# Performance work log

Measured on AMD Instinct MI355X. Metric: run time of the kernel, lower is better.

The kernel has to match this reference:

```python
import jax, jax.numpy as jnp
import numpy as np

D, H, B, NSTEPS = 128, 512, 128, 16


def setup_inputs() -> dict:
    key = jax.random.key(0)
    k0, k1, k2, k3 = jax.random.split(key, 4)
    s1 = 1.0 / np.sqrt(D)
    s2 = 0.1 / np.sqrt(H)  # small output scale keeps the flow well-conditioned
    return {
        "x0": jax.random.normal(k0, (B, D), jnp.float32),
        "W1": jax.random.normal(k1, (D, H), jnp.float32) * s1,
        "b1": jnp.zeros((H,), jnp.float32),
        "u1": jax.random.normal(k2, (H,), jnp.float32) * 0.1,
        "W2": jax.random.normal(k3, (H, D), jnp.float32) * s2,
        "b2": jnp.zeros((D,), jnp.float32),
        "n_steps": NSTEPS,
    }


def reference(x0, W1, b1, u1, W2, b2, n_steps):
    d = x0.shape[-1]
    LOG2PI = float(np.log(2.0 * np.pi))
    # log prob of x0 under standard-normal prior p0
    log_px0 = -0.5 * jnp.sum(x0 * x0, axis=-1) - 0.5 * d * LOG2PI
    dt = 1.0 / n_steps

    sg = jax.lax.stop_gradient
    W1s, b1s, u1s, W2s, b2s = sg(W1), sg(b1), sg(u1), sg(W2), sg(b2)

    def vf(t, x, w1, c1, v1, w2, c2):  # time-conditioned MLP vector field, x: (d,)
        return jnp.tanh(x @ w1 + c1 + t * v1) @ w2 + c2

    eye = jnp.eye(d, dtype=x0.dtype)

    def f_single(t, x):
        # exact Jacobian trace via vmapped JVP over identity tangents (stop-grad params)
        apply_sg = lambda xx: vf(t, xx, W1s, b1s, u1s, W2s, b2s)
        jvp1 = lambda e: jax.jvp(apply_sg, (x,), (e,))[1]
        jac = jax.vmap(jvp1)(eye)              # (d, d)
        dxdt = vf(t, x, W1, b1, u1, W2, b2)    # with grad-carrying params
        dlogpxdt = -jnp.trace(jac)
        gradlogpx = -x                          # grad log of standard-normal target
        dkldt = -jnp.vdot(gradlogpx, dxdt) + dlogpxdt
        return dxdt, dlogpxdt, dkldt

    rhs = jax.vmap(f_single, in_axes=(None, 0))  # batch over samples

    # Dopri5 Butcher tableau (fixed-step 5th-order solution)
    A = (
        (1 / 5,),
        (3 / 40, 9 / 40),
        (44 / 45, -56 / 15, 32 / 9),
        (19372 / 6561, -25360 / 2187, 64448 / 6561, -212 / 729),
        (9017 / 3168, -355 / 33, 46732 / 5247, 49 / 176, -5103 / 18656),
    )
    C = (1 / 5, 3 / 10, 4 / 5, 8 / 9, 1.0)
    BW = (35 / 384, 0.0, 500 / 1113, 125 / 192, -2187 / 6784, 11 / 84)

    def lin(y, ks, cs):  # y + dt * sum(c_i * k_i), tree-structured state
        return jax.tree_util.tree_map(
            lambda yv, *kv: yv + dt * sum(c * k for c, k in zip(cs, kv)), y, *ks)

    def step(y, t):
        ks = [rhs(t, y[0])]
        for ai, ci in zip(A, C):
            yi = lin(y, ks, ai)
            ks.append(rhs(t + ci * dt, yi[0]))
        return lin(y, ks, BW), None

    nb = x0.shape[0]
    y0 = (x0, jnp.zeros((nb,), x0.dtype), jnp.zeros((nb,), x0.dtype))
    ts = jnp.arange(n_steps, dtype=x0.dtype) * dt
    (z, log_det, kl), _ = jax.lax.scan(step, y0, ts)
    log_px = log_px0 + log_det
    return z, log_px, kl
```

## Files before the change

### kernel.cpp

```cpp
#include <hip/hip_runtime.h>

#define TPB 512

typedef _Float16 hf2 __attribute__((ext_vector_type(2)));

__device__ __forceinline__ hf2 as_h2(unsigned u) { return __builtin_bit_cast(hf2, u); }
__device__ __forceinline__ unsigned pk2h(float a, float b) {
    unsigned la = (unsigned)__builtin_bit_cast(unsigned short, (_Float16)a);
    unsigned hb = (unsigned)__builtin_bit_cast(unsigned short, (_Float16)b);
    return la | (hb << 16);
}
__device__ __forceinline__ unsigned short h16(float a) {
    return __builtin_bit_cast(unsigned short, (_Float16)a);
}
#define FDOT2(w, x, acc) __builtin_amdgcn_fdot2(as_h2(w), as_h2(x), (acc), false)

__device__ __forceinline__ unsigned rdl(unsigned v, int l) {
    return (unsigned)__builtin_amdgcn_readlane((int)v, l);
}

#define G16(M) M(0) M(1) M(2) M(3) M(4) M(5) M(6) M(7) M(8) M(9) M(10) M(11) \
  M(12) M(13) M(14) M(15)

#define RED64(v) { v += __shfl_xor(v,32,64); v += __shfl_xor(v,16,64); \
  v += __shfl_xor(v,8,64); v += __shfl_xor(v,4,64); v += __shfl_xor(v,2,64); \
  v += __shfl_xor(v,1,64); }

__global__ __launch_bounds__(TPB, 1) void vi_node_kernel(
    const float* __restrict__ x0, const float* __restrict__ W1,
    const float* __restrict__ b1, const float* __restrict__ u1,
    const float* __restrict__ W2, const float* __restrict__ b2,
    const int* __restrict__ nsp, float* __restrict__ out, int nB)
{
    const int s    = blockIdx.x;
    const int t    = threadIdx.x;
    const int j    = t & 127;
    const int q    = t >> 7;
    const int kb   = q << 7;
    const int lane = t & 63;
    const int wid  = t >> 6;

    __shared__ uint4 W1L[16 * 512];
    __shared__ __align__(16) float    xs32[128];
    __shared__ __align__(8)  unsigned xsPK[64];
    __shared__ __align__(16) float    ys[128];
    __shared__ __align__(8)  unsigned aPK[256];
    __shared__ __align__(16) float    part[4][128];
    __shared__ __align__(16) float    kx[6][128];
    __shared__ float wredT[2][6][8];
    __shared__ float wredX[2][6][2];
    __shared__ float sqred[2];

#pragma unroll
    for (int c = 0; c < 16; ++c) {
        const float* gp = W1 + (8 * c) * 512 + t;
        uint4 wv;
        wv.x = pk2h(gp[0],        gp[512]);
        wv.y = pk2h(gp[2 * 512],  gp[3 * 512]);
        wv.z = pk2h(gp[4 * 512],  gp[5 * 512]);
        wv.w = pk2h(gp[6 * 512],  gp[7 * 512]);
        W1L[c * 512 + t] = wv;
    }

#define DECLZ(g) unsigned z_##g##_0, z_##g##_1, z_##g##_2, z_##g##_3;
    G16(DECLZ)
#define PKW2(r) pk2h(W2[(r) * 128 + j], W2[((r) + 1) * 128 + j])
#define LOADZ(g) { const int r_ = kb + 8 * (g); \
    z_##g##_0 = PKW2(r_);     z_##g##_1 = PKW2(r_ + 2); \
    z_##g##_2 = PKW2(r_ + 4); z_##g##_3 = PKW2(r_ + 6); }
    G16(LOADZ)

    const float b1k = b1[t];
    const float u1k = u1[t];
    const float b2j = b2[j];

    const int ns = nsp[0];
    const float dt = 1.f / (float)ns;

    if (t < 128) {
        float xv0 = x0[s * 128 + t];
        ys[t] = xv0;
        xs32[t] = xv0;
        ((unsigned short*)xsPK)[t] = h16(xv0);
        float sq = xv0 * xv0;
        RED64(sq)
        if (lane == 0) sqred[wid] = sq;
    }
    __syncthreads();

    float wd = 0.f;
    {
        const float4* w2r4 = (const float4*)(W2 + t * 128);
#pragma unroll
        for (int c = 0; c < 16; ++c) {
            uint4 wv = W1L[c * 512 + t];
            float4 a4 = w2r4[2 * c], b4 = w2r4[2 * c + 1];
            wd = FDOT2(wv.x, pk2h(a4.x, a4.y), wd);
            wd = FDOT2(wv.y, pk2h(a4.z, a4.w), wd);
            wd = FDOT2(wv.z, pk2h(b4.x, b4.y), wd);
            wd = FDOT2(wv.w, pk2h(b4.z, b4.w), wd);
        }
    }
    const float sumsq = sqred[0] + sqred[1];
    float ld_acc = 0.f, kl_acc = 0.f;

#define H4(c) { uint4 w_ = W1L[(c) * 512 + t]; \
    m0 = FDOT2(w_.x, rdl(xv, 4*(c)+0), m0); \
    m1 = FDOT2(w_.y, rdl(xv, 4*(c)+1), m1); \
    m2 = FDOT2(w_.z, rdl(xv, 4*(c)+2), m2); \
    m3 = FDOT2(w_.w, rdl(xv, 4*(c)+3), m3); }

#define P4(g) { \
    p0 = FDOT2(z_##g##_0, rdl(av, 4*(g)+0), p0); \
    p1 = FDOT2(z_##g##_1, rdl(av, 4*(g)+1), p1); \
    p2 = FDOT2(z_##g##_2, rdl(av, 4*(g)+2), p2); \
    p3 = FDOT2(z_##g##_3, rdl(av, 4*(g)+3), p3); }

#define K(sidx) kx[sidx][t]

#define EVAL(STAGE, TVAL, XNEW, EXTRA)                                         \
    {                                                                          \
        const unsigned xv = xsPK[lane];            \
        float m0 = 0.f, m1 = 0.f, m2 = 0.f, m3 = 0.f;                          \
        H4(0) H4(1) H4(2) H4(3) H4(4) H4(5) H4(6) H4(7)                        \
        H4(8) H4(9) H4(10) H4(11) H4(12) H4(13) H4(14) H4(15)                  \
        float hh = fmaf((TVAL), u1k, b1k) + ((m0 + m1) + (m2 + m3));           \
        float ee = __expf(2.f * hh);                                           \
        float aa = 1.f - 2.f / (ee + 1.f);                           \
        ((unsigned short*)aPK)[t] = h16(aa);                                   \
        float trp = (1.f - aa * aa) * wd;                                      \
        RED64(trp)                                                             \
        if (lane == 0) wredT[par][STAGE][wid] = trp;                           \
        __syncthreads();                            \
        const unsigned av = aPK[(q << 6) + lane];   \
        float p0 = 0.f, p1 = 0.f, p2 = 0.f, p3 = 0.f;                          \
        P4(0) P4(1) P4(2) P4(3) P4(4) P4(5) P4(6) P4(7)                        \
        P4(8) P4(9) P4(10) P4(11) P4(12) P4(13) P4(14) P4(15)                  \
        part[q][j] = (p0 + p1) + (p2 + p3);                                    \
        __syncthreads();                               \
        if (t < 128) {                                                         \
            float dx = ((part[0][t] + part[1][t]) + (part[2][t] + part[3][t])) \
                       + b2j;                                                  \
            kx[STAGE][t] = dx;                                                 \
            float xd = xs32[t] * dx;                                           \
            RED64(xd)                                                          \
            if (lane == 0) wredX[par][STAGE][wid] = xd;                        \
            float xnew = (XNEW);                                               \
            xs32[t] = xnew;                                                    \
            ((unsigned short*)xsPK)[t] = h16(xnew);                            \
            EXTRA                                                              \
        }                                                                      \
        __syncthreads();                               \
    }

    for (int n = 0; n < ns; ++n) {
        const float tn = (float)n;
        const int par = n & 1;

        EVAL(0, dt * tn,
             fmaf(dt, 0.2f * dx, ys[t]), ;)

        EVAL(1, dt * (tn + 0.2f),
             ys[t] + dt * (0.075f * K(0) + 0.225f * dx), ;)

        EVAL(2, dt * (tn + 0.3f),
             ys[t] + dt * ((float)(44.0/45.0)  * K(0) + (float)(-56.0/15.0) * K(1)
                         + (float)(32.0/9.0)   * dx), ;)

        EVAL(3, dt * (tn + 0.8f),
             ys[t] + dt * ((float)(19372.0/6561.0) * K(0) + (float)(-25360.0/2187.0) * K(1)
                         + (float)(64448.0/6561.0) * K(2) + (float)(-212.0/729.0)    * dx), ;)

        EVAL(4, dt * (tn + (float)(8.0/9.0)),
             ys[t] + dt * ((float)(9017.0/3168.0)  * K(0) + (float)(-355.0/33.0)     * K(1)
                         + (float)(46732.0/5247.0) * K(2) + (float)(49.0/176.0)      * K(3)
                         + (float)(-5103.0/18656.0)* dx), ;)

        EVAL(5, dt * (tn + 1.0f),
             ys[t] + dt * ((float)(35.0/384.0)     * K(0) + (float)(500.0/1113.0)   * K(2)
                         + (float)(125.0/192.0)    * K(3) + (float)(-2187.0/6784.0) * K(4)
                         + (float)(11.0/84.0)      * dx),
             ys[t] = xnew;)

        if (t == 0) {
#define TAILS(sidx, bw) { \
            float tr_ = ((wredT[par][sidx][0] + wredT[par][sidx][1])  \
                       + (wredT[par][sidx][2] + wredT[par][sidx][3])) \
                      + ((wredT[par][sidx][4] + wredT[par][sidx][5])  \
                       + (wredT[par][sidx][6] + wredT[par][sidx][7])); \
            float dv_ = wredX[par][sidx][0] + wredX[par][sidx][1]; \
            ld_acc += dt * (bw) * (-tr_); \
            kl_acc += dt * (bw) * (dv_ - tr_); }
            TAILS(0, (float)(35.0/384.0))
            TAILS(2, (float)(500.0/1113.0))
            TAILS(3, (float)(125.0/192.0))
            TAILS(4, (float)(-2187.0/6784.0))
            TAILS(5, (float)(11.0/84.0))
        }
    }

    if (t < 128) out[s * 128 + t] = ys[t];
    if (t == 0) {
        const float LOG2PI = 1.8378770664093454f;
        float lpx0 = -0.5f * sumsq - 0.5f * 128.f * LOG2PI;
        out[nB * 128 + s]      = lpx0 + ld_acc;
        out[nB * 128 + nB + s] = kl_acc;
    }
}

extern "C" void kernel_launch(void* const* d_in, const int* in_sizes, int n_in,
                              void* d_out, int out_size, void* d_ws, size_t ws_size,
                              hipStream_t stream) {
    const float* x0 = (const float*)d_in[0];
    const float* W1 = (const float*)d_in[1];
    const float* b1 = (const float*)d_in[2];
    const float* u1 = (const float*)d_in[3];
    const float* W2 = (const float*)d_in[4];
    const float* b2 = (const float*)d_in[5];
    const int*  nsp = (const int*)d_in[6];
    float* out = (float*)d_out;
    const int nB = in_sizes[0] / 128;

    hipLaunchKernelGGL(vi_node_kernel, dim3(nB), dim3(TPB), 0, stream,
                       x0, W1, b1, u1, W2, b2, nsp, out, nB);
}
```

Measured before the change: 255.6 us.

## Double block size and split matvec reductions across wave halves with LDS vector reads

The block grows from 512 to 1024 threads. Each hidden unit's W1 dot product is split across two half-waves and combined with a cross-lane shuffle. The W2 product is spread over 8 partial slices instead of 4, which halves the register-held W2 fragment per thread. Broadcast operands now come from vectorized LDS uint4 reads instead of scalar readlane, aiming to shorten the serial dependent chain in each stage. In exchange, only half the lanes do the tanh work, and there are more partial sums to combine and larger barriers.

Result: faster. 237.9 us (-6.9%).

```diff
diff --git a/kernel.cpp b/kernel.cpp
--- a/kernel.cpp
+++ b/kernel.cpp
@@ -1,6 +1,6 @@
 #include <hip/hip_runtime.h>
 
-#define TPB 512
+#define TPB 1024
 
 typedef _Float16 hf2 __attribute__((ext_vector_type(2)));
 
@@ -15,12 +15,7 @@
 }
 #define FDOT2(w, x, acc) __builtin_amdgcn_fdot2(as_h2(w), as_h2(x), (acc), false)
 
-__device__ __forceinline__ unsigned rdl(unsigned v, int l) {
-    return (unsigned)__builtin_amdgcn_readlane((int)v, l);
-}
-
-#define G16(M) M(0) M(1) M(2) M(3) M(4) M(5) M(6) M(7) M(8) M(9) M(10) M(11) \
-  M(12) M(13) M(14) M(15)
+#define G8(M) M(0) M(1) M(2) M(3) M(4) M(5) M(6) M(7)
 
 #define RED64(v) { v += __shfl_xor(v,32,64); v += __shfl_xor(v,16,64); \
   v += __shfl_xor(v,8,64); v += __shfl_xor(v,4,64); v += __shfl_xor(v,2,64); \
@@ -34,44 +29,51 @@
 {
     const int s    = blockIdx.x;
     const int t    = threadIdx.x;
+    const int l    = t & 63;
+    const int w    = t >> 6;
+    const int h    = 32 * w + (t & 31);
+    const int half = (t >> 5) & 1;
+    const int hb   = half * 32;
     const int j    = t & 127;
     const int q    = t >> 7;
-    const int kb   = q << 7;
-    const int lane = t & 63;
-    const int wid  = t >> 6;
 
     __shared__ uint4 W1L[16 * 512];
     __shared__ __align__(16) float    xs32[128];
-    __shared__ __align__(8)  unsigned xsPK[64];
+    __shared__ __align__(16) unsigned xsPK[64];
     __shared__ __align__(16) float    ys[128];
-    __shared__ __align__(8)  unsigned aPK[256];
-    __shared__ __align__(16) float    part[4][128];
+    __shared__ __align__(16) unsigned aPK[256];
+    __shared__ __align__(16) float    part[8][128];
     __shared__ __align__(16) float    kx[6][128];
-    __shared__ float wredT[2][6][8];
+    __shared__ float wredT[2][6][16];
     __shared__ float wredX[2][6][2];
     __shared__ float sqred[2];
 
+    {
+        const int col = t & 511;
+        const int c0  = t >> 9;
 #pragma unroll
-    for (int c = 0; c < 16; ++c) {
-        const float* gp = W1 + (8 * c) * 512 + t;
-        uint4 wv;
-        wv.x = pk2h(gp[0],        gp[512]);
-        wv.y = pk2h(gp[2 * 512],  gp[3 * 512]);
-        wv.z = pk2h(gp[4 * 512],  gp[5 * 512]);
-        wv.w = pk2h(gp[6 * 512],  gp[7 * 512]);
-        W1L[c * 512 + t] = wv;
-    }
-
-#define DECLZ(g) unsigned z_##g##_0, z_##g##_1, z_##g##_2, z_##g##_3;
-    G16(DECLZ)
+        for (int cc = 0; cc < 8; ++cc) {
+            const int c = 8 * c0 + cc;
+            const float* gp = W1 + (8 * c) * 512 + col;
+            uint4 wv;
+            wv.x = pk2h(gp[0],        gp[512]);
+            wv.y = pk2h(gp[2 * 512],  gp[3 * 512]);
+            wv.z = pk2h(gp[4 * 512],  gp[5 * 512]);
+            wv.w = pk2h(gp[6 * 512],  gp[7 * 512]);
+            W1L[c * 512 + col] = wv;
+        }
+    }
+
+#define DECLZ(cc) unsigned zc_##cc##_0, zc_##cc##_1, zc_##cc##_2, zc_##cc##_3;
+    G8(DECLZ)
 #define PKW2(r) pk2h(W2[(r) * 128 + j], W2[((r) + 1) * 128 + j])
-#define LOADZ(g) { const int r_ = kb + 8 * (g); \
-    z_##g##_0 = PKW2(r_);     z_##g##_1 = PKW2(r_ + 2); \
-    z_##g##_2 = PKW2(r_ + 4); z_##g##_3 = PKW2(r_ + 6); }
-    G16(LOADZ)
-
-    const float b1k = b1[t];
-    const float u1k = u1[t];
+#define LOADZ(cc) { const int r_ = 64 * q + 8 * (cc); \
+    zc_##cc##_0 = PKW2(r_);     zc_##cc##_1 = PKW2(r_ + 2); \
+    zc_##cc##_2 = PKW2(r_ + 4); zc_##cc##_3 = PKW2(r_ + 6); }
+    G8(LOADZ)
+
+    const float b1k = b1[h];
+    const float u1k = u1[h];
     const float b2j = b2[j];
 
     const int ns = nsp[0];
@@ -84,67 +86,70 @@
         ((unsigned short*)xsPK)[t] = h16(xv0);
         float sq = xv0 * xv0;
         RED64(sq)
-        if (lane == 0) sqred[wid] = sq;
+        if (l == 0) sqred[w] = sq;
     }
     __syncthreads();
 
-    float wd = 0.f;
+    float wd;
     {
-        const float4* w2r4 = (const float4*)(W2 + t * 128);
+        float wp = 0.f;
+        const float4* w2r4 = (const float4*)(W2 + h * 128);
 #pragma unroll
-        for (int c = 0; c < 16; ++c) {
-            uint4 wv = W1L[c * 512 + t];
-            float4 a4 = w2r4[2 * c], b4 = w2r4[2 * c + 1];
-            wd = FDOT2(wv.x, pk2h(a4.x, a4.y), wd);
-            wd = FDOT2(wv.y, pk2h(a4.z, a4.w), wd);
-            wd = FDOT2(wv.z, pk2h(b4.x, b4.y), wd);
-            wd = FDOT2(wv.w, pk2h(b4.z, b4.w), wd);
+        for (int cc = 0; cc < 8; ++cc) {
+            uint4 wv = W1L[(8 * half + cc) * 512 + h];
+            float4 a4 = w2r4[16 * half + 2 * cc];
+            float4 b4 = w2r4[16 * half + 2 * cc + 1];
+            wp = FDOT2(wv.x, pk2h(a4.x, a4.y), wp);
+            wp = FDOT2(wv.y, pk2h(a4.z, a4.w), wp);
+            wp = FDOT2(wv.z, pk2h(b4.x, b4.y), wp);
+            wp = FDOT2(wv.w, pk2h(b4.z, b4.w), wp);
         }
+        wd = wp + __shfl_xor(wp, 32, 64);
     }
     const float sumsq = sqred[0] + sqred[1];
     float ld_acc = 0.f, kl_acc = 0.f;
 
-#define H4(c) { uint4 w_ = W1L[(c) * 512 + t]; \
-    m0 = FDOT2(w_.x, rdl(xv, 4*(c)+0), m0); \
-    m1 = FDOT2(w_.y, rdl(xv, 4*(c)+1), m1); \
-    m2 = FDOT2(w_.z, rdl(xv, 4*(c)+2), m2); \
-    m3 = FDOT2(w_.w, rdl(xv, 4*(c)+3), m3); }
-
-#define P4(g) { \
-    p0 = FDOT2(z_##g##_0, rdl(av, 4*(g)+0), p0); \
-    p1 = FDOT2(z_##g##_1, rdl(av, 4*(g)+1), p1); \
-    p2 = FDOT2(z_##g##_2, rdl(av, 4*(g)+2), p2); \
-    p3 = FDOT2(z_##g##_3, rdl(av, 4*(g)+3), p3); }
+#define H4(cc) { uint4 w_ = W1L[(8 * half + (cc)) * 512 + h]; \
+    const uint4 xu_ = *(const uint4*)&xsPK[hb + 4 * (cc)];  \
+    m0 = FDOT2(w_.x, xu_.x, m0); m1 = FDOT2(w_.y, xu_.y, m1); \
+    m2 = FDOT2(w_.z, xu_.z, m2); m3 = FDOT2(w_.w, xu_.w, m3); }
+
+#define P4(cc) { const uint4 av_ = *(const uint4*)&aPK[32 * q + 4 * (cc)];  \
+    p0 = FDOT2(zc_##cc##_0, av_.x, p0); p1 = FDOT2(zc_##cc##_1, av_.y, p1); \
+    p2 = FDOT2(zc_##cc##_2, av_.z, p2); p3 = FDOT2(zc_##cc##_3, av_.w, p3); }
 
 #define K(sidx) kx[sidx][t]
 
 #define EVAL(STAGE, TVAL, XNEW, EXTRA)                                         \
     {                                                                          \
-        const unsigned xv = xsPK[lane];            \
         float m0 = 0.f, m1 = 0.f, m2 = 0.f, m3 = 0.f;                          \
-        H4(0) H4(1) H4(2) H4(3) H4(4) H4(5) H4(6) H4(7)                        \
-        H4(8) H4(9) H4(10) H4(11) H4(12) H4(13) H4(14) H4(15)                  \
-        float hh = fmaf((TVAL), u1k, b1k) + ((m0 + m1) + (m2 + m3));           \
-        float ee = __expf(2.f * hh);                                           \
-        float aa = 1.f - 2.f / (ee + 1.f);                           \
-        ((unsigned short*)aPK)[t] = h16(aa);                                   \
-        float trp = (1.f - aa * aa) * wd;                                      \
-        RED64(trp)                                                             \
-        if (lane == 0) wredT[par][STAGE][wid] = trp;                           \
+        G8(H4)                                                                 \
+        float mm = (m0 + m1) + (m2 + m3);                                      \
+        mm += __shfl_xor(mm, 32, 64);              \
+        if ((t & 32) == 0) {                       \
+            float hh = fmaf((TVAL), u1k, b1k) + mm;                            \
+            float ee = __expf(2.f * hh);                                       \
+            float aa = 1.f - 2.f / (ee + 1.f);                       \
+            ((unsigned short*)aPK)[h] = h16(aa);                               \
+            float trp = (1.f - aa * aa) * wd;                                  \
+            trp += __shfl_xor(trp, 16, 64); trp += __shfl_xor(trp, 8, 64);     \
+            trp += __shfl_xor(trp, 4, 64);  trp += __shfl_xor(trp, 2, 64);     \
+            trp += __shfl_xor(trp, 1, 64);                                     \
+            if (l == 0) wredT[par][STAGE][w] = trp;                            \
+        }                                                                      \
         __syncthreads();                            \
-        const unsigned av = aPK[(q << 6) + lane];   \
         float p0 = 0.f, p1 = 0.f, p2 = 0.f, p3 = 0.f;                          \
-        P4(0) P4(1) P4(2) P4(3) P4(4) P4(5) P4(6) P4(7)                        \
-        P4(8) P4(9) P4(10) P4(11) P4(12) P4(13) P4(14) P4(15)                  \
+        G8(P4)                                                                 \
         part[q][j] = (p0 + p1) + (p2 + p3);                                    \
         __syncthreads();                               \
         if (t < 128) {                                                         \
-            float dx = ((part[0][t] + part[1][t]) + (part[2][t] + part[3][t])) \
+            float dx = (((part[0][t] + part[1][t]) + (part[2][t] + part[3][t]))\
+                      + ((part[4][t] + part[5][t]) + (part[6][t] + part[7][t])))\
                        + b2j;                                                  \
             kx[STAGE][t] = dx;                                                 \
             float xd = xs32[t] * dx;                                           \
             RED64(xd)                                                          \
-            if (lane == 0) wredX[par][STAGE][wid] = xd;                        \
+            if (l == 0) wredX[par][STAGE][w] = xd;                             \
             float xnew = (XNEW);                                               \
             xs32[t] = xnew;                                                    \
             ((unsigned short*)xsPK)[t] = h16(xnew);                            \
@@ -184,11 +189,10 @@
 
         if (t == 0) {
 #define TAILS(sidx, bw) { \
-            float tr_ = ((wredT[par][sidx][0] + wredT[par][sidx][1])  \
-                       + (wredT[par][sidx][2] + wredT[par][sidx][3])) \
-                      + ((wredT[par][sidx][4] + wredT[par][sidx][5])  \
-                       + (wredT[par][sidx][6] + wredT[par][sidx][7])); \
-            float dv_ = wredX[par][sidx][0] + wredX[par][sidx][1]; \
+            float tr_ = 0.f, dv_; \
+            _Pragma("unroll") \
+            for (int ww = 0; ww < 16; ++ww) tr_ += wredT[par][sidx][ww]; \
+            dv_ = wredX[par][sidx][0] + wredX[par][sidx][1]; \
             ld_acc += dt * (bw) * (-tr_); \
             kl_acc += dt * (bw) * (dv_ - tr_); }
             TAILS(0, (float)(35.0/384.0))
```
